# Kernel tuning notes

Hardware: AMD Instinct MI355X
Metric: run time of the kernel (lower is better)

Reference implementation:

```python
import jax, jax.numpy as jnp
import numpy as np

D_MODEL = 1024
NHEAD = 16
D_K = D_MODEL // NHEAD


def setup_inputs() -> dict:
    key = jax.random.key(0)
    ks = jax.random.split(key, 9)
    s = 1.0 / np.sqrt(D_MODEL)
    return {
        "x": jax.random.normal(ks[0], (4, 2048, D_MODEL), dtype=jnp.float32),
        "Wq": jax.random.uniform(ks[1], (D_MODEL, D_MODEL), jnp.float32, -s, s),
        "bq": jax.random.uniform(ks[2], (D_MODEL,), jnp.float32, -s, s),
        "Wk": jax.random.uniform(ks[3], (D_MODEL, D_MODEL), jnp.float32, -s, s),
        "bk": jax.random.uniform(ks[4], (D_MODEL,), jnp.float32, -s, s),
        "Wv": jax.random.uniform(ks[5], (D_MODEL, D_MODEL), jnp.float32, -s, s),
        "bv": jax.random.uniform(ks[6], (D_MODEL,), jnp.float32, -s, s),
        "Wo": jax.random.uniform(ks[7], (D_MODEL, D_MODEL), jnp.float32, -s, s),
        "bo": jax.random.uniform(ks[8], (D_MODEL,), jnp.float32, -s, s),
    }


def reference(x, Wq, bq, Wk, bk, Wv, bv, Wo, bo):
    B, S, D = x.shape
    H, dk = NHEAD, D_K

    def split_heads(t):  # [B,S,D] -> [B,H,S,dk]
        return t.reshape(B, S, H, dk).transpose(0, 2, 1, 3)

    q = split_heads(x @ Wq + bq)
    k = split_heads(x @ Wk + bk)
    v = split_heads(x @ Wv + bv)

    scores = jnp.einsum('bhqd,bhkd->bhqk', q, k) / jnp.sqrt(jnp.float32(dk))
    attn = jax.nn.softmax(scores, axis=-1)
    out = jnp.einsum('bhqk,bhkd->bhqd', attn, v)  # [B,H,S,dk]
    out = out.transpose(0, 2, 1, 3).reshape(B, S, D)
    return out @ Wo + bo
```

## Files before the change

kernel.cpp:

```cpp
#include <hip/hip_runtime.h>


typedef short short8 __attribute__((ext_vector_type(8)));
typedef float f32x4 __attribute__((ext_vector_type(4)));
typedef float f32x16 __attribute__((ext_vector_type(16)));

#define DMODEL 1024
#define NH 16
#define DK 64
#define SEQ 2048
#define NB 4
#define MTOT (NB*SEQ)
#define KSCALE 0.18033688f

__device__ __forceinline__ unsigned short f2bf(float f) {
    union { float f; unsigned u; } v; v.f = f;
    unsigned r = (v.u + 0x7FFFu + ((v.u >> 16) & 1u)) >> 16;
    return (unsigned short)r;
}

__device__ __forceinline__ unsigned pk2(float a, float b) {
    unsigned r;
    asm("v_cvt_pk_bf16_f32 %0, %1, %2" : "=v"(r) : "v"(a), "v"(b));
    return r;
}

__device__ __forceinline__ float exp2a(float x) {
    float r; asm("v_exp_f32 %0, %1" : "=v"(r) : "v"(x)); return r;
}

__device__ __forceinline__ float max3a(float a, float b, float c) {
    float r; asm("v_max3_f32 %0, %1, %2, %3" : "=v"(r) : "v"(a), "v"(b), "v"(c)); return r;
}

__device__ __forceinline__ void plswap(unsigned &a, unsigned &b) {
    asm volatile("v_permlane32_swap_b32 %0, %1" : "+v"(a), "+v"(b));
}

__device__ __forceinline__ void gload16(const short* g, short* l) {
    __builtin_amdgcn_global_load_lds(
        (const __attribute__((address_space(1))) unsigned*)(const void*)g,
        (__attribute__((address_space(3))) unsigned*)(void*)l,
        16, 0, 0);
}

__device__ __forceinline__ void vm4()    { asm volatile("s_waitcnt vmcnt(4)"    ::: "memory"); }
__device__ __forceinline__ void vm0()    { asm volatile("s_waitcnt vmcnt(0)"    ::: "memory"); }
__device__ __forceinline__ void lgkm8()  { asm volatile("s_waitcnt lgkmcnt(8)"  ::: "memory"); }
__device__ __forceinline__ void lgkm0()  { asm volatile("s_waitcnt lgkmcnt(0)"  ::: "memory"); }

union Frag { short8 s8; unsigned u[4]; };

#define NCVT (MTOT * DMODEL / 4 / 256)
__global__ __launch_bounds__(256) void prep_kernel(
    const float* __restrict__ x, short* __restrict__ xb,
    const float* __restrict__ Wq, const float* __restrict__ Wk,
    const float* __restrict__ Wv, const float* __restrict__ Wo,
    short* __restrict__ Wqkvt, short* __restrict__ Wot)
{
    __shared__ float t[32][33];
    int bid = blockIdx.x;
    if (bid < NCVT) {
        int i = bid * 256 + threadIdx.x;
        float4 v = ((const float4*)x)[i];
        short4 o;
        o.x = (short)f2bf(v.x); o.y = (short)f2bf(v.y);
        o.z = (short)f2bf(v.z); o.w = (short)f2bf(v.w);
        ((short4*)xb)[i] = o;
        return;
    }
    int wb = bid - NCVT;
    int widx = wb >> 10, tile = wb & 1023;
    const float* W = (widx == 0) ? Wq : (widx == 1) ? Wk : (widx == 2) ? Wv : Wo;
    short* dst = (widx < 3) ? (Wqkvt + (size_t)widx * DMODEL * DMODEL) : Wot;
    int r0 = (tile >> 5) * 32, c0 = (tile & 31) * 32;
    int tr = threadIdx.x >> 3;
    int tc = (threadIdx.x & 7) * 4;
    float4 v = *(const float4*)&W[(r0 + tr) * DMODEL + c0 + tc];
    t[tr][tc + 0] = v.x; t[tr][tc + 1] = v.y; t[tr][tc + 2] = v.z; t[tr][tc + 3] = v.w;
    __syncthreads();
    short4 o;
    o.x = (short)f2bf(t[tc + 0][tr]);
    o.y = (short)f2bf(t[tc + 1][tr]);
    o.z = (short)f2bf(t[tc + 2][tr]);
    o.w = (short)f2bf(t[tc + 3][tr]);
    *(short4*)&dst[(c0 + tr) * DMODEL + r0 + tc] = o;
}

template<int MODE>
__global__ __launch_bounds__(256) void gemm_kernel(
    const short* __restrict__ A, const short* __restrict__ Bt,
    const float* __restrict__ b0, const float* __restrict__ b1, const float* __restrict__ b2,
    short* __restrict__ Qb, short* __restrict__ Kb, short* __restrict__ Vtb,
    float* __restrict__ Cout)
{
    __shared__ __align__(16) short L[3][2][128 * 32];
    const int K = DMODEL;
    const int NHP = 2 * (K / 64);
    int m0 = blockIdx.y * 128, n0 = blockIdx.x * 128;
    int tid = threadIdx.x, lane = tid & 63, wid = tid >> 6;
    int wm = (wid >> 1) * 64, wn = (wid & 1) * 64;

    int srowl = (lane >> 2);
    int scoll = ((lane & 3) ^ ((lane >> 3) & 3)) * 8;
    const short* aSrc = A + (size_t)(m0 + wid * 32 + srowl) * K + scoll;
    const short* bSrc = Bt + (size_t)(n0 + wid * 32 + srowl) * K + scoll;

    f32x4 acc[4][4];
    #pragma unroll
    for (int i = 0; i < 4; i++)
        #pragma unroll
        for (int j = 0; j < 4; j++) acc[i][j] = (f32x4){0.f, 0.f, 0.f, 0.f};

    auto STAGE = [&](int H) {
        int sl = H % 3;
        const short* as = aSrc + H * 32;
        const short* bs = bSrc + H * 32;
        #pragma unroll
        for (int i = 0; i < 2; ++i) {
            gload16(as + (size_t)i * 16 * K, &L[sl][0][(wid * 32 + i * 16) * 32]);
            gload16(bs + (size_t)i * 16 * K, &L[sl][1][(wid * 32 + i * 16) * 32]);
        }
    };
    auto LDA = [&](int sl, short8* f) {
        #pragma unroll
        for (int m = 0; m < 4; m++) {
            int r = wm + m * 16 + (lane & 15);
            f[m] = *(const short8*)&L[sl][0][r * 32 + (((lane >> 4) ^ ((r >> 1) & 3)) * 8)];
        }
    };
    auto LDB = [&](int sl, short8* f) {
        #pragma unroll
        for (int n = 0; n < 4; n++) {
            int r = wn + n * 16 + (lane & 15);
            f[n] = *(const short8*)&L[sl][1][r * 32 + (((lane >> 4) ^ ((r >> 1) & 3)) * 8)];
        }
    };

    short8 fa0[4], fb0[4], fa1[4], fb1[4];

    STAGE(0);
    STAGE(1);
    vm4();
    __builtin_amdgcn_s_barrier();
    LDA(0, fa0); LDB(0, fb0);

    #pragma unroll
    for (int H = 0; H < NHP; ++H) {
        short8* curA = (H & 1) ? fa1 : fa0;
        short8* curB = (H & 1) ? fb1 : fb0;
        short8* nxtA = (H & 1) ? fa0 : fa1;
        short8* nxtB = (H & 1) ? fb0 : fb1;

        if (H + 2 < NHP) { STAGE(H + 2); vm4(); }
        else             { vm0(); }
        __builtin_amdgcn_s_barrier();

        if (H + 1 < NHP) { LDA((H + 1) % 3, nxtA); LDB((H + 1) % 3, nxtB); lgkm8(); }
        else             { lgkm0(); }
        __builtin_amdgcn_s_barrier();
        __builtin_amdgcn_sched_barrier(0);

        __builtin_amdgcn_s_setprio(1);
        #pragma unroll
        for (int i = 0; i < 4; i++)
            #pragma unroll
            for (int j = 0; j < 4; j++)
                acc[i][j] = __builtin_amdgcn_mfma_f32_16x16x32_bf16(curA[i], curB[j], acc[i][j], 0, 0, 0);
        __builtin_amdgcn_s_setprio(0);
    }

    #pragma unroll
    for (int i = 0; i < 4; i++) {
        #pragma unroll
        for (int j = 0; j < 4; j++) {
            int col = n0 + wn + j * 16 + (lane & 15);
            #pragma unroll
            for (int r = 0; r < 4; r++) {
                int row = m0 + wm + i * 16 + (lane >> 4) * 4 + r;
                float v = acc[i][j][r];
                if (MODE == 0) {
                    int seg = col >> 10, c = col & 1023;
                    const float* bp = (seg == 0) ? b0 : (seg == 1 ? b1 : b2);
                    v += bp[c];
                    if (seg == 1) v *= KSCALE;
                    unsigned short bv = f2bf(v);
                    int hh = c >> 6, d = c & 63, bb = row >> 11, s = row & 2047;
                    if (seg == 0)      Qb [(((bb * NH + hh) * SEQ) + s) * DK + d] = (short)bv;
                    else if (seg == 1) Kb [(((bb * NH + hh) * SEQ) + s) * DK + d] = (short)bv;
                    else               Vtb[(((bb * NH + hh) * DK) + d) * SEQ + s] = (short)bv;
                } else {
                    Cout[row * DMODEL + col] = v + b0[col];
                }
            }
        }
    }
}

__global__ __launch_bounds__(256) void attn_kernel(
    const short* __restrict__ Qb, const short* __restrict__ Kb,
    const short* __restrict__ Vtb, short* __restrict__ AOb)
{
    __shared__ __align__(16) short Ks[64 * 64];
    __shared__ __align__(16) short Vs[64 * 64];
    char* ksb = (char*)Ks;
    char* vsb = (char*)Vs;

    int bid = blockIdx.x;
    int wk = (bid & 7) * 128 + (bid >> 3);
    int qi = wk & 15, bh = wk >> 4;
    int h = bh & (NH - 1), b = bh >> 4;
    int q0 = qi * 128;

    int tid = threadIdx.x, lane = tid & 63, wid = tid >> 6;
    int hi = lane >> 5, l31 = lane & 31, l7 = lane & 7;
    const short* Qp = Qb + (size_t)bh * SEQ * DK;
    const short* Kp = Kb + (size_t)bh * SEQ * DK;
    const short* Vp = Vtb + (size_t)bh * DK * SEQ;

    short8 qf[4];
    #pragma unroll
    for (int ks = 0; ks < 4; ks++)
        qf[ks] = *(const short8*)&Qp[(q0 + wid * 32 + l31) * DK + ks * 16 + hi * 8];

    Frag onef;
    onef.u[0] = 0x3F803F80u; onef.u[1] = 0x3F803F80u;
    onef.u[2] = 0x3F803F80u; onef.u[3] = 0x3F803F80u;
    short8 onesv = onef.s8;

    f32x16 ot0, ot1, ot2;
    #pragma unroll
    for (int r = 0; r < 16; r++) { ot0[r] = 0.f; ot1[r] = 0.f; ot2[r] = 0.f; }
    float mrun = 0.f;

    int srow = tid >> 3, ssl = tid & 7;
    #pragma unroll
    for (int i = 0; i < 2; i++) {
        int row = srow + 32 * i;
        *(short8*)(ksb + ((row * 128 + ssl * 16) ^ ((row & 7) << 4))) =
            *(const short8*)&Kp[row * DK + ssl * 8];
        *(short8*)(vsb + ((row * 128 + ssl * 16) ^ ((row & 7) << 4))) =
            *(const short8*)&Vp[row * SEQ + ssl * 8];
    }
    __syncthreads();

    const int NT = SEQ / 64;
    for (int t = 0; t < NT; ++t) {
        short8 nk[2], nv[2];
        if (t + 1 < NT) {
            int kv0n = (t + 1) * 64;
            #pragma unroll
            for (int i = 0; i < 2; i++) {
                int row = srow + 32 * i;
                nk[i] = *(const short8*)&Kp[(kv0n + row) * DK + ssl * 8];
                nv[i] = *(const short8*)&Vp[row * SEQ + kv0n + ssl * 8];
            }
        }

        float negm = -mrun;
        f32x16 st0, st1;
        #pragma unroll
        for (int r = 0; r < 16; r++) { st0[r] = negm; st1[r] = negm; }
        __builtin_amdgcn_s_setprio(1);
        #pragma unroll
        for (int ks = 0; ks < 4; ks++) {
            short8 kf0 = *(const short8*)(ksb + ((l31 * 128 + ks * 32 + hi * 16) ^ (l7 << 4)));
            short8 kf1 = *(const short8*)(ksb + (((32 + l31) * 128 + ks * 32 + hi * 16) ^ (l7 << 4)));
            st0 = __builtin_amdgcn_mfma_f32_32x32x16_bf16(kf0, qf[ks], st0, 0, 0, 0);
            st1 = __builtin_amdgcn_mfma_f32_32x32x16_bf16(kf1, qf[ks], st1, 0, 0, 0);
        }
        __builtin_amdgcn_s_setprio(0);

        float m8[8];
        #pragma unroll
        for (int i = 0; i < 8; i++) m8[i] = max3a(st0[i], st0[i + 8], st1[i]);
        float m4[4];
        #pragma unroll
        for (int i = 0; i < 4; i++) m4[i] = max3a(m8[i], m8[i + 4], st1[i + 8]);
        float m2a = max3a(m4[0], m4[2], st1[12]);
        float m2b = max3a(m4[1], m4[3], st1[13]);
        float mxv = max3a(m2a, m2b, st1[14]);
        mxv = fmaxf(mxv, st1[15]);
        float mt = fmaxf(mxv, __shfl_xor(mxv, 32, 64));

        if (!__all(mt <= 11.0f)) {
            float d = fmaxf(mt, 0.f);
            float al = exp2a(-d);
            ot2[0] *= al;
            #pragma unroll
            for (int r = 0; r < 16; r++) {
                ot0[r] *= al; ot1[r] *= al;
                st0[r] -= d; st1[r] -= d;
            }
            mrun += d;
        }
        #pragma unroll
        for (int r = 0; r < 16; r++) {
            st0[r] = exp2a(st0[r]);
            st1[r] = exp2a(st1[r]);
        }

        unsigned w0[8], w1[8];
        #pragma unroll
        for (int m = 0; m < 4; m++) {
            w0[m * 2]     = pk2(st0[4 * m], st0[4 * m + 1]);
            w0[m * 2 + 1] = pk2(st0[4 * m + 2], st0[4 * m + 3]);
            w1[m * 2]     = pk2(st1[4 * m], st1[4 * m + 1]);
            w1[m * 2 + 1] = pk2(st1[4 * m + 2], st1[4 * m + 3]);
        }
        short8 pf[4];
        #pragma unroll
        for (int ks = 0; ks < 4; ks++) {
            unsigned a0 = (ks < 2) ? w0[4 * (ks & 1) + 0] : w1[4 * (ks & 1) + 0];
            unsigned b0_ = (ks < 2) ? w0[4 * (ks & 1) + 2] : w1[4 * (ks & 1) + 2];
            unsigned a1 = (ks < 2) ? w0[4 * (ks & 1) + 1] : w1[4 * (ks & 1) + 1];
            unsigned b1_ = (ks < 2) ? w0[4 * (ks & 1) + 3] : w1[4 * (ks & 1) + 3];
            plswap(a0, b0_);
            plswap(a1, b1_);
            Frag f;
            f.u[0] = a0; f.u[1] = a1; f.u[2] = b0_; f.u[3] = b1_;
            pf[ks] = f.s8;
        }

        __builtin_amdgcn_s_setprio(1);
        #pragma unroll
        for (int ks = 0; ks < 4; ks++) {
            short8 vf0 = *(const short8*)(vsb + ((l31 * 128 + ks * 32 + hi * 16) ^ (l7 << 4)));
            short8 vf1 = *(const short8*)(vsb + (((32 + l31) * 128 + ks * 32 + hi * 16) ^ (l7 << 4)));
            ot0 = __builtin_amdgcn_mfma_f32_32x32x16_bf16(vf0, pf[ks], ot0, 0, 0, 0);
            ot1 = __builtin_amdgcn_mfma_f32_32x32x16_bf16(vf1, pf[ks], ot1, 0, 0, 0);
            ot2 = __builtin_amdgcn_mfma_f32_32x32x16_bf16(onesv, pf[ks], ot2, 0, 0, 0);
        }
        __builtin_amdgcn_s_setprio(0);

        __syncthreads();
        if (t + 1 < NT) {
            #pragma unroll
            for (int i = 0; i < 2; i++) {
                int row = srow + 32 * i;
                *(short8*)(ksb + ((row * 128 + ssl * 16) ^ ((row & 7) << 4))) = nk[i];
                *(short8*)(vsb + ((row * 128 + ssl * 16) ^ ((row & 7) << 4))) = nv[i];
            }
        }
        __syncthreads();
    }

    float inv = 1.f / ot2[0];
    int srow_q = b * SEQ + q0 + wid * 32 + l31;
    short* outp = AOb + (size_t)srow_q * DMODEL + h * DK;
    #pragma unroll
    for (int g = 0; g < 4; g++) {
        int d0 = 8 * g + 4 * hi;
        uint2 u;
        u.x = pk2(ot0[4 * g] * inv, ot0[4 * g + 1] * inv);
        u.y = pk2(ot0[4 * g + 2] * inv, ot0[4 * g + 3] * inv);
        *(uint2*)&outp[d0] = u;
        uint2 v2;
        v2.x = pk2(ot1[4 * g] * inv, ot1[4 * g + 1] * inv);
        v2.y = pk2(ot1[4 * g + 2] * inv, ot1[4 * g + 3] * inv);
        *(uint2*)&outp[32 + d0] = v2;
    }
}

extern "C" void kernel_launch(void* const* d_in, const int* in_sizes, int n_in,
                              void* d_out, int out_size, void* d_ws, size_t ws_size,
                              hipStream_t stream)
{
    const float* x  = (const float*)d_in[0];
    const float* Wq = (const float*)d_in[1];
    const float* bq = (const float*)d_in[2];
    const float* Wk = (const float*)d_in[3];
    const float* bk = (const float*)d_in[4];
    const float* Wv = (const float*)d_in[5];
    const float* bv = (const float*)d_in[6];
    const float* Wo = (const float*)d_in[7];
    const float* bo = (const float*)d_in[8];
    float* out = (float*)d_out;

    char* w = (char*)d_ws;
    short* xb    = (short*)w; w += (size_t)MTOT * DMODEL * 2;
    short* Wqkvt = (short*)w; w += (size_t)3 * DMODEL * DMODEL * 2;
    short* Wot   = (short*)w; w += (size_t)DMODEL * DMODEL * 2;
    short* Qb    = (short*)w; w += (size_t)MTOT * DMODEL * 2;
    short* Kb    = (short*)w; w += (size_t)MTOT * DMODEL * 2;
    short* Vtb   = (short*)w; w += (size_t)MTOT * DMODEL * 2;
    short* AOb   = (short*)w; w += (size_t)MTOT * DMODEL * 2;

    prep_kernel<<<NCVT + 4096, 256, 0, stream>>>(x, xb, Wq, Wk, Wv, Wo, Wqkvt, Wot);

    gemm_kernel<0><<<dim3(3 * DMODEL / 128, MTOT / 128), 256, 0, stream>>>(
        xb, Wqkvt, bq, bk, bv, Qb, Kb, Vtb, nullptr);

    attn_kernel<<<dim3(SEQ / 128 * NH * NB), 256, 0, stream>>>(Qb, Kb, Vtb, AOb);

    gemm_kernel<1><<<dim3(DMODEL / 128, MTOT / 128), 256, 0, stream>>>(
        AOb, Wot, bo, nullptr, nullptr, nullptr, nullptr, nullptr, out);
}
```

Measured before the change: 238.5 us.

## Process 64 query rows per wave in attention, replace ones-MFMA row sum with VALU reduction

Each wave now handles two 32-row query tiles (256 queries per block), so each K/V tile loaded into LDS and each K/V fragment read feeds twice as many MFMAs. The row-sum denominator, previously computed by an extra MFMA against a ones vector, is now accumulated with VALU adds and a cross-half shuffle. The grid halves to 512 blocks, and the running max starts at -1e30 and is tracked per tile instead of pre-subtracted in the accumulator init. This raises register pressure (four score and four output accumulators) and halves the number of blocks, which may reduce occupancy and load balance across CUs.

```diff
diff --git a/kernel.cpp b/kernel.cpp
--- a/kernel.cpp
+++ b/kernel.cpp
@@ -207,10 +207,10 @@
     char* vsb = (char*)Vs;
 
     int bid = blockIdx.x;
-    int wk = (bid & 7) * 128 + (bid >> 3);
-    int qi = wk & 15, bh = wk >> 4;
+    int wk = (bid & 7) * 64 + (bid >> 3);
+    int qi = wk & 7, bh = wk >> 3;
     int h = bh & (NH - 1), b = bh >> 4;
-    int q0 = qi * 128;
+    int q0 = qi * 256;
 
     int tid = threadIdx.x, lane = tid & 63, wid = tid >> 6;
     int hi = lane >> 5, l31 = lane & 31, l7 = lane & 7;
@@ -218,20 +218,18 @@
     const short* Kp = Kb + (size_t)bh * SEQ * DK;
     const short* Vp = Vtb + (size_t)bh * DK * SEQ;
 
-    short8 qf[4];
-    #pragma unroll
-    for (int ks = 0; ks < 4; ks++)
-        qf[ks] = *(const short8*)&Qp[(q0 + wid * 32 + l31) * DK + ks * 16 + hi * 8];
-
-    Frag onef;
-    onef.u[0] = 0x3F803F80u; onef.u[1] = 0x3F803F80u;
-    onef.u[2] = 0x3F803F80u; onef.u[3] = 0x3F803F80u;
-    short8 onesv = onef.s8;
-
-    f32x16 ot0, ot1, ot2;
-    #pragma unroll
-    for (int r = 0; r < 16; r++) { ot0[r] = 0.f; ot1[r] = 0.f; ot2[r] = 0.f; }
-    float mrun = 0.f;
+    int qbase = q0 + wid * 64;
+    short8 qfA[4], qfB[4];
+    #pragma unroll
+    for (int ks = 0; ks < 4; ks++) {
+        qfA[ks] = *(const short8*)&Qp[(qbase + l31) * DK + ks * 16 + hi * 8];
+        qfB[ks] = *(const short8*)&Qp[(qbase + 32 + l31) * DK + ks * 16 + hi * 8];
+    }
+
+    f32x16 oA0, oA1, oB0, oB1;
+    #pragma unroll
+    for (int r = 0; r < 16; r++) { oA0[r] = 0.f; oA1[r] = 0.f; oB0[r] = 0.f; oB1[r] = 0.f; }
+    float mrunA = -1e30f, lrunA = 0.f, mrunB = -1e30f, lrunB = 0.f;
 
     int srow = tid >> 3, ssl = tid & 7;
     #pragma unroll
@@ -257,69 +255,131 @@
             }
         }
 
-        float negm = -mrun;
-        f32x16 st0, st1;
-        #pragma unroll
-        for (int r = 0; r < 16; r++) { st0[r] = negm; st1[r] = negm; }
+        f32x16 sA0, sA1, sB0, sB1;
+        #pragma unroll
+        for (int r = 0; r < 16; r++) { sA0[r] = 0.f; sA1[r] = 0.f; sB0[r] = 0.f; sB1[r] = 0.f; }
         __builtin_amdgcn_s_setprio(1);
         #pragma unroll
         for (int ks = 0; ks < 4; ks++) {
             short8 kf0 = *(const short8*)(ksb + ((l31 * 128 + ks * 32 + hi * 16) ^ (l7 << 4)));
             short8 kf1 = *(const short8*)(ksb + (((32 + l31) * 128 + ks * 32 + hi * 16) ^ (l7 << 4)));
-            st0 = __builtin_amdgcn_mfma_f32_32x32x16_bf16(kf0, qf[ks], st0, 0, 0, 0);
-            st1 = __builtin_amdgcn_mfma_f32_32x32x16_bf16(kf1, qf[ks], st1, 0, 0, 0);
+            sA0 = __builtin_amdgcn_mfma_f32_32x32x16_bf16(kf0, qfA[ks], sA0, 0, 0, 0);
+            sA1 = __builtin_amdgcn_mfma_f32_32x32x16_bf16(kf1, qfA[ks], sA1, 0, 0, 0);
+            sB0 = __builtin_amdgcn_mfma_f32_32x32x16_bf16(kf0, qfB[ks], sB0, 0, 0, 0);
+            sB1 = __builtin_amdgcn_mfma_f32_32x32x16_bf16(kf1, qfB[ks], sB1, 0, 0, 0);
         }
         __builtin_amdgcn_s_setprio(0);
 
-        float m8[8];
-        #pragma unroll
-        for (int i = 0; i < 8; i++) m8[i] = max3a(st0[i], st0[i + 8], st1[i]);
-        float m4[4];
-        #pragma unroll
-        for (int i = 0; i < 4; i++) m4[i] = max3a(m8[i], m8[i + 4], st1[i + 8]);
-        float m2a = max3a(m4[0], m4[2], st1[12]);
-        float m2b = max3a(m4[1], m4[3], st1[13]);
-        float mxv = max3a(m2a, m2b, st1[14]);
-        mxv = fmaxf(mxv, st1[15]);
-        float mt = fmaxf(mxv, __shfl_xor(mxv, 32, 64));
-
-        if (!__all(mt <= 11.0f)) {
-            float d = fmaxf(mt, 0.f);
-            float al = exp2a(-d);
-            ot2[0] *= al;
+        short8 pfA[4], pfB[4];
+        {
+            float m8[8];
+            #pragma unroll
+            for (int i = 0; i < 8; i++) m8[i] = max3a(sA0[i], sA0[i + 8], sA1[i]);
+            float m4[4];
+            #pragma unroll
+            for (int i = 0; i < 4; i++) m4[i] = max3a(m8[i], m8[i + 4], sA1[i + 8]);
+            float m2a = max3a(m4[0], m4[2], sA1[12]);
+            float m2b = max3a(m4[1], m4[3], sA1[13]);
+            float mxv = max3a(m2a, m2b, sA1[14]);
+            mxv = fmaxf(mxv, sA1[15]);
+            float mt = fmaxf(mxv, __shfl_xor(mxv, 32, 64));
+            if (!__all(mt - mrunA <= 11.0f)) {
+                float mn = fmaxf(mrunA, mt);
+                float al = exp2a(mrunA - mn);
+                lrunA *= al;
+                #pragma unroll
+                for (int r = 0; r < 16; r++) { oA0[r] *= al; oA1[r] *= al; }
+                mrunA = mn;
+            }
             #pragma unroll
             for (int r = 0; r < 16; r++) {
-                ot0[r] *= al; ot1[r] *= al;
-                st0[r] -= d; st1[r] -= d;
-            }
-            mrun += d;
-        }
-        #pragma unroll
-        for (int r = 0; r < 16; r++) {
-            st0[r] = exp2a(st0[r]);
-            st1[r] = exp2a(st1[r]);
-        }
-
-        unsigned w0[8], w1[8];
-        #pragma unroll
-        for (int m = 0; m < 4; m++) {
-            w0[m * 2]     = pk2(st0[4 * m], st0[4 * m + 1]);
-            w0[m * 2 + 1] = pk2(st0[4 * m + 2], st0[4 * m + 3]);
-            w1[m * 2]     = pk2(st1[4 * m], st1[4 * m + 1]);
-            w1[m * 2 + 1] = pk2(st1[4 * m + 2], st1[4 * m + 3]);
-        }
-        short8 pf[4];
-        #pragma unroll
-        for (int ks = 0; ks < 4; ks++) {
-            unsigned a0 = (ks < 2) ? w0[4 * (ks & 1) + 0] : w1[4 * (ks & 1) + 0];
-            unsigned b0_ = (ks < 2) ? w0[4 * (ks & 1) + 2] : w1[4 * (ks & 1) + 2];
-            unsigned a1 = (ks < 2) ? w0[4 * (ks & 1) + 1] : w1[4 * (ks & 1) + 1];
-            unsigned b1_ = (ks < 2) ? w0[4 * (ks & 1) + 3] : w1[4 * (ks & 1) + 3];
-            plswap(a0, b0_);
-            plswap(a1, b1_);
-            Frag f;
-            f.u[0] = a0; f.u[1] = a1; f.u[2] = b0_; f.u[3] = b1_;
-            pf[ks] = f.s8;
+                sA0[r] = exp2a(sA0[r] - mrunA);
+                sA1[r] = exp2a(sA1[r] - mrunA);
+            }
+            float s16[16];
+            #pragma unroll
+            for (int r = 0; r < 16; r++) s16[r] = sA0[r] + sA1[r];
+            #pragma unroll
+            for (int s = 8; s > 0; s >>= 1)
+                #pragma unroll
+                for (int r = 0; r < 8; r++) if (r < s) s16[r] += s16[r + s];
+            lrunA += s16[0] + __shfl_xor(s16[0], 32, 64);
+
+            unsigned w0[8], w1[8];
+            #pragma unroll
+            for (int m = 0; m < 4; m++) {
+                w0[m * 2]     = pk2(sA0[4 * m], sA0[4 * m + 1]);
+                w0[m * 2 + 1] = pk2(sA0[4 * m + 2], sA0[4 * m + 3]);
+                w1[m * 2]     = pk2(sA1[4 * m], sA1[4 * m + 1]);
+                w1[m * 2 + 1] = pk2(sA1[4 * m + 2], sA1[4 * m + 3]);
+            }
+            #pragma unroll
+            for (int ks = 0; ks < 4; ks++) {
+                unsigned a0 = (ks < 2) ? w0[4 * (ks & 1) + 0] : w1[4 * (ks & 1) + 0];
+                unsigned b0_ = (ks < 2) ? w0[4 * (ks & 1) + 2] : w1[4 * (ks & 1) + 2];
+                unsigned a1 = (ks < 2) ? w0[4 * (ks & 1) + 1] : w1[4 * (ks & 1) + 1];
+                unsigned b1_ = (ks < 2) ? w0[4 * (ks & 1) + 3] : w1[4 * (ks & 1) + 3];
+                plswap(a0, b0_);
+                plswap(a1, b1_);
+                Frag f;
+                f.u[0] = a0; f.u[1] = a1; f.u[2] = b0_; f.u[3] = b1_;
+                pfA[ks] = f.s8;
+            }
+        }
+        {
+            float m8[8];
+            #pragma unroll
+            for (int i = 0; i < 8; i++) m8[i] = max3a(sB0[i], sB0[i + 8], sB1[i]);
+            float m4[4];
+            #pragma unroll
+            for (int i = 0; i < 4; i++) m4[i] = max3a(m8[i], m8[i + 4], sB1[i + 8]);
+            float m2a = max3a(m4[0], m4[2], sB1[12]);
+            float m2b = max3a(m4[1], m4[3], sB1[13]);
+            float mxv = max3a(m2a, m2b, sB1[14]);
+            mxv = fmaxf(mxv, sB1[15]);
+            float mt = fmaxf(mxv, __shfl_xor(mxv, 32, 64));
+            if (!__all(mt - mrunB <= 11.0f)) {
+                float mn = fmaxf(mrunB, mt);
+                float al = exp2a(mrunB - mn);
+                lrunB *= al;
+                #pragma unroll
+                for (int r = 0; r < 16; r++) { oB0[r] *= al; oB1[r] *= al; }
+                mrunB = mn;
+            }
+            #pragma unroll
+            for (int r = 0; r < 16; r++) {
+                sB0[r] = exp2a(sB0[r] - mrunB);
+                sB1[r] = exp2a(sB1[r] - mrunB);
+            }
+            float s16[16];
+            #pragma unroll
+            for (int r = 0; r < 16; r++) s16[r] = sB0[r] + sB1[r];
+            #pragma unroll
+            for (int s = 8; s > 0; s >>= 1)
+                #pragma unroll
+                for (int r = 0; r < 8; r++) if (r < s) s16[r] += s16[r + s];
+            lrunB += s16[0] + __shfl_xor(s16[0], 32, 64);
+
+            unsigned w0[8], w1[8];
+            #pragma unroll
+            for (int m = 0; m < 4; m++) {
+                w0[m * 2]     = pk2(sB0[4 * m], sB0[4 * m + 1]);
+                w0[m * 2 + 1] = pk2(sB0[4 * m + 2], sB0[4 * m + 3]);
+                w1[m * 2]     = pk2(sB1[4 * m], sB1[4 * m + 1]);
+                w1[m * 2 + 1] = pk2(sB1[4 * m + 2], sB1[4 * m + 3]);
+            }
+            #pragma unroll
+            for (int ks = 0; ks < 4; ks++) {
+                unsigned a0 = (ks < 2) ? w0[4 * (ks & 1) + 0] : w1[4 * (ks & 1) + 0];
+                unsigned b0_ = (ks < 2) ? w0[4 * (ks & 1) + 2] : w1[4 * (ks & 1) + 2];
+                unsigned a1 = (ks < 2) ? w0[4 * (ks & 1) + 1] : w1[4 * (ks & 1) + 1];
+                unsigned b1_ = (ks < 2) ? w0[4 * (ks & 1) + 3] : w1[4 * (ks & 1) + 3];
+                plswap(a0, b0_);
+                plswap(a1, b1_);
+                Frag f;
+                f.u[0] = a0; f.u[1] = a1; f.u[2] = b0_; f.u[3] = b1_;
+                pfB[ks] = f.s8;
+            }
         }
 
         __builtin_amdgcn_s_setprio(1);
@@ -327,9 +387,10 @@
         for (int ks = 0; ks < 4; ks++) {
             short8 vf0 = *(const short8*)(vsb + ((l31 * 128 + ks * 32 + hi * 16) ^ (l7 << 4)));
             short8 vf1 = *(const short8*)(vsb + (((32 + l31) * 128 + ks * 32 + hi * 16) ^ (l7 << 4)));
-            ot0 = __builtin_amdgcn_mfma_f32_32x32x16_bf16(vf0, pf[ks], ot0, 0, 0, 0);
-            ot1 = __builtin_amdgcn_mfma_f32_32x32x16_bf16(vf1, pf[ks], ot1, 0, 0, 0);
-            ot2 = __builtin_amdgcn_mfma_f32_32x32x16_bf16(onesv, pf[ks], ot2, 0, 0, 0);
+            oA0 = __builtin_amdgcn_mfma_f32_32x32x16_bf16(vf0, pfA[ks], oA0, 0, 0, 0);
+            oA1 = __builtin_amdgcn_mfma_f32_32x32x16_bf16(vf1, pfA[ks], oA1, 0, 0, 0);
+            oB0 = __builtin_amdgcn_mfma_f32_32x32x16_bf16(vf0, pfB[ks], oB0, 0, 0, 0);
+            oB1 = __builtin_amdgcn_mfma_f32_32x32x16_bf16(vf1, pfB[ks], oB1, 0, 0, 0);
         }
         __builtin_amdgcn_s_setprio(0);
 
@@ -345,20 +406,39 @@
         __syncthreads();
     }
 
-    float inv = 1.f / ot2[0];
-    int srow_q = b * SEQ + q0 + wid * 32 + l31;
-    short* outp = AOb + (size_t)srow_q * DMODEL + h * DK;
-    #pragma unroll
-    for (int g = 0; g < 4; g++) {
-        int d0 = 8 * g + 4 * hi;
-        uint2 u;
-        u.x = pk2(ot0[4 * g] * inv, ot0[4 * g + 1] * inv);
-        u.y = pk2(ot0[4 * g + 2] * inv, ot0[4 * g + 3] * inv);
-        *(uint2*)&outp[d0] = u;
-        uint2 v2;
-        v2.x = pk2(ot1[4 * g] * inv, ot1[4 * g + 1] * inv);
-        v2.y = pk2(ot1[4 * g + 2] * inv, ot1[4 * g + 3] * inv);
-        *(uint2*)&outp[32 + d0] = v2;
+    {
+        float inv = 1.f / lrunA;
+        int srow_q = b * SEQ + qbase + l31;
+        short* outp = AOb + (size_t)srow_q * DMODEL + h * DK;
+        #pragma unroll
+        for (int g = 0; g < 4; g++) {
+            int d0 = 8 * g + 4 * hi;
+            uint2 u;
+            u.x = pk2(oA0[4 * g] * inv, oA0[4 * g + 1] * inv);
+            u.y = pk2(oA0[4 * g + 2] * inv, oA0[4 * g + 3] * inv);
+            *(uint2*)&outp[d0] = u;
+            uint2 v2;
+            v2.x = pk2(oA1[4 * g] * inv, oA1[4 * g + 1] * inv);
+            v2.y = pk2(oA1[4 * g + 2] * inv, oA1[4 * g + 3] * inv);
+            *(uint2*)&outp[32 + d0] = v2;
+        }
+    }
+    {
+        float inv = 1.f / lrunB;
+        int srow_q = b * SEQ + qbase + 32 + l31;
+        short* outp = AOb + (size_t)srow_q * DMODEL + h * DK;
+        #pragma unroll
+        for (int g = 0; g < 4; g++) {
+            int d0 = 8 * g + 4 * hi;
+            uint2 u;
+            u.x = pk2(oB0[4 * g] * inv, oB0[4 * g + 1] * inv);
+            u.y = pk2(oB0[4 * g + 2] * inv, oB0[4 * g + 3] * inv);
+            *(uint2*)&outp[d0] = u;
+            uint2 v2;
+            v2.x = pk2(oB1[4 * g] * inv, oB1[4 * g + 1] * inv);
+            v2.y = pk2(oB1[4 * g + 2] * inv, oB1[4 * g + 3] * inv);
+            *(uint2*)&outp[32 + d0] = v2;
+        }
     }
 }
 
@@ -391,7 +471,7 @@
     gemm_kernel<0><<<dim3(3 * DMODEL / 128, MTOT / 128), 256, 0, stream>>>(
         xb, Wqkvt, bq, bk, bv, Qb, Kb, Vtb, nullptr);
 
-    attn_kernel<<<dim3(SEQ / 128 * NH * NB), 256, 0, stream>>>(Qb, Kb, Vtb, AOb);
+    attn_kernel<<<dim3(SEQ / 256 * NH * NB), 256, 0, stream>>>(Qb, Kb, Vtb, AOb);
 
     gemm_kernel<1><<<dim3(DMODEL / 128, MTOT / 128), 256, 0, stream>>>(
         AOb, Wot, bo, nullptr, nullptr, nullptr, nullptr, nullptr, out);
```

New measurement: 263.7 us. 10.6% more time.
